# Optimization experiments

Hardware: AMD Instinct MI355X
Metric: run time of the kernel (lower is better)

Reference implementation:

```python
import jax, jax.numpy as jnp
import numpy as np

NUM_HEADS = 16


def setup_inputs() -> dict:
    key = jax.random.key(0)
    ks = jax.random.split(key, 5)
    B, N, D = 2, 2048, 1024
    scale = 1.0 / np.sqrt(D)  # roughly xavier-ish magnitude for weights
    return {
        "x": jax.random.normal(ks[0], (B, N, D), dtype=jnp.float32),
        "W_query": jax.random.normal(ks[1], (D, D), dtype=jnp.float32) * scale,
        "W_key": jax.random.normal(ks[2], (D, D), dtype=jnp.float32) * scale,
        "W_value": jax.random.normal(ks[3], (D, D), dtype=jnp.float32) * scale,
        "W_output": jax.random.normal(ks[4], (D, D), dtype=jnp.float32) * scale,
    }


def reference(x, W_query, W_key, W_value, W_output):
    # x: [B, N, D]; weights: [D, D]
    B, N, D = x.shape
    H = NUM_HEADS
    hd = D // H

    def mh_embed(W):
        # linear_embedding then split heads: [B, N, D] -> [B, H, N, hd]
        y = jnp.einsum("bnd,de->bne", x, W)
        return y.reshape(B, N, H, hd).transpose(0, 2, 1, 3)

    q = mh_embed(W_query)
    k = mh_embed(W_key)
    v = mh_embed(W_value)

    # NOTE: source scales by token_dim**-0.5 (full model dim), not head_dim
    attn = jnp.einsum("bhnd,bhmd->bhnm", q, k) * (D ** -0.5)
    attn = jax.nn.softmax(attn, axis=-1)
    out = jnp.einsum("bhnm,bhmd->bhnd", attn, v)  # [B, H, N, hd]

    out = out.transpose(0, 2, 1, 3).reshape(B, N, D)  # merge heads
    out = jnp.einsum("bnd,de->bne", out, W_output)
    return out
```

## Files before the change

kernel.cpp:

```cpp
#include <hip/hip_runtime.h>

#define D_MODEL 1024
#define N_TOK   2048
#define NHEAD   16
#define HDIM    64
#define BATCH   2
#define M_TOT   (BATCH*N_TOK)

typedef unsigned short u16;
typedef __bf16 bf16x8 __attribute__((ext_vector_type(8)));
typedef float  f32x4  __attribute__((ext_vector_type(4)));

#define QSCALE 0.04508422002777439f

__device__ __forceinline__ u16 f2bf(float f) {
  union { float f; unsigned u; } v; v.f = f;
  unsigned r = v.u + 0x7fffu + ((v.u >> 16) & 1u);
  return (u16)(r >> 16);
}

__device__ __forceinline__ unsigned pk2bf(float a, float b) {
#if __has_builtin(__builtin_amdgcn_cvt_pk_bf16_f32)
  typedef __bf16 bf16x2_t __attribute__((ext_vector_type(2)));
  bf16x2_t r = __builtin_amdgcn_cvt_pk_bf16_f32(a, b);
  union { bf16x2_t v; unsigned u; } c; c.v = r; return c.u;
#else
  return (unsigned)f2bf(a) | ((unsigned)f2bf(b) << 16);
#endif
}

__device__ __forceinline__ void gl2lds16(const void* g, void* l) {
  __builtin_amdgcn_global_load_lds(
      (__attribute__((address_space(1))) void*)g,
      (__attribute__((address_space(3))) void*)l, 16, 0, 0);
}

__global__ void prep_kernel(const float* __restrict__ x,
                            const float* __restrict__ s0, const float* __restrict__ s1,
                            const float* __restrict__ s2, const float* __restrict__ s3,
                            u16* __restrict__ xb,
                            u16* __restrict__ d0, u16* __restrict__ d1,
                            u16* __restrict__ d2, u16* __restrict__ d3) {
  const int t = threadIdx.y * 32 + threadIdx.x;
  if (blockIdx.z == 4) {
    int base = (blockIdx.y * 32 + blockIdx.x) * 256 + t;
#pragma unroll
    for (int r = 0; r < 4; ++r) {
      int i = base + r * 262144;
      float4 v = ((const float4*)x)[i];
      ushort4 o;
      o.x = f2bf(v.x); o.y = f2bf(v.y); o.z = f2bf(v.z); o.w = f2bf(v.w);
      ((ushort4*)xb)[i] = o;
    }
    return;
  }
  const float* src; u16* dst;
  switch (blockIdx.z) {
    case 0:  src = s0; dst = d0; break;
    case 1:  src = s1; dst = d1; break;
    case 2:  src = s2; dst = d2; break;
    default: src = s3; dst = d3; break;
  }
  float sc = (blockIdx.z == 0) ? QSCALE : 1.0f;
  __shared__ float tile[32][33];
  int xg = blockIdx.x * 32 + threadIdx.x;
  int ybase = blockIdx.y * 32;
#pragma unroll
  for (int r = 0; r < 4; ++r)
    tile[threadIdx.y + r*8][threadIdx.x] = src[(size_t)(ybase + threadIdx.y + r*8)*D_MODEL + xg];
  __syncthreads();
#pragma unroll
  for (int r = 0; r < 4; ++r)
    dst[(size_t)(blockIdx.x*32 + threadIdx.y + r*8)*D_MODEL + ybase + threadIdx.x] =
        f2bf(tile[threadIdx.x][threadIdx.y + r*8] * sc);
}

__device__ __forceinline__ void gemm_body(const u16* __restrict__ A,
                                          const u16* __restrict__ Bt,
                                          void* __restrict__ Cout, int mode) {
  __shared__ __attribute__((aligned(16))) u16 lA[2][128*32];
  __shared__ __attribute__((aligned(16))) u16 lB[2][128*32];
  const int t = threadIdx.x;
  const int lane = t & 63, w = t >> 6;
  const int wm = w >> 1, wn = w & 1;
  const int q4 = lane >> 4, l15 = lane & 15;
  const int m0 = blockIdx.y * 128, n0 = blockIdx.x * 128;

  const int c0 = t, c1 = 256 + t;
  const int r0 = c0 >> 2, g0 = (c0 & 3) ^ (r0 & 3);
  const int r1 = c1 >> 2, g1 = (c1 & 3) ^ (r1 & 3);

  f32x4 acc[4][4] = {};

  gl2lds16(A  + (size_t)(m0 + r0)*D_MODEL + g0*8, &lA[0][c0*8]);
  gl2lds16(Bt + (size_t)(n0 + r0)*D_MODEL + g0*8, &lB[0][c0*8]);
  gl2lds16(A  + (size_t)(m0 + r1)*D_MODEL + g1*8, &lA[0][c1*8]);
  gl2lds16(Bt + (size_t)(n0 + r1)*D_MODEL + g1*8, &lB[0][c1*8]);

  for (int it = 0; it < 32; ++it) {
    const int cur = it & 1;
    __syncthreads();
    if (it + 1 < 32) {
      const int kn = (it + 1) * 32;
      u16* dA = &lA[cur ^ 1][0]; u16* dB = &lB[cur ^ 1][0];
      gl2lds16(A  + (size_t)(m0 + r0)*D_MODEL + kn + g0*8, dA + c0*8);
      gl2lds16(Bt + (size_t)(n0 + r0)*D_MODEL + kn + g0*8, dB + c0*8);
      gl2lds16(A  + (size_t)(m0 + r1)*D_MODEL + kn + g1*8, dA + c1*8);
      gl2lds16(Bt + (size_t)(n0 + r1)*D_MODEL + kn + g1*8, dB + c1*8);
    }
    const u16* sA = &lA[cur][0]; const u16* sB = &lB[cur][0];
    bf16x8 af[4], bfr[4];
#pragma unroll
    for (int mi = 0; mi < 4; ++mi) {
      int r = wm*64 + mi*16 + l15;
      af[mi] = *(const bf16x8*)(sA + r*32 + ((q4 ^ (r & 3)) * 8));
    }
#pragma unroll
    for (int ni = 0; ni < 4; ++ni) {
      int r = wn*64 + ni*16 + l15;
      bfr[ni] = *(const bf16x8*)(sB + r*32 + ((q4 ^ (r & 3)) * 8));
    }
#pragma unroll
    for (int mi = 0; mi < 4; ++mi)
#pragma unroll
      for (int ni = 0; ni < 4; ++ni)
        acc[mi][ni] = __builtin_amdgcn_mfma_f32_16x16x32_bf16(af[mi], bfr[ni], acc[mi][ni], 0, 0, 0);
  }

#pragma unroll
  for (int mi = 0; mi < 4; ++mi) {
#pragma unroll
    for (int ni = 0; ni < 4; ++ni) {
      const int tok0 = m0 + wm*64 + mi*16 + q4*4;
      const int col  = n0 + wn*64 + ni*16 + l15;
      if (mode == 0) {
        u16* D = (u16*)Cout;
#pragma unroll
        for (int r = 0; r < 4; ++r) {
          int tok = tok0 + r;
          int b = tok >> 11, n = tok & (N_TOK-1);
          int h = col >> 6, d = col & (HDIM-1);
          D[(((size_t)(b*NHEAD + h))*N_TOK + n)*HDIM + d] = f2bf(acc[mi][ni][r]);
        }
      } else if (mode == 2) {
        int b = tok0 >> 11, n = tok0 & (N_TOK-1);
        int h = col >> 6, d = col & (HDIM-1);
        ushort4 pk;
        pk.x = f2bf(acc[mi][ni][0]); pk.y = f2bf(acc[mi][ni][1]);
        pk.z = f2bf(acc[mi][ni][2]); pk.w = f2bf(acc[mi][ni][3]);
        *(ushort4*)((u16*)Cout + ((size_t)(b*NHEAD + h)*HDIM + d)*N_TOK + n) = pk;
      } else {
        float* D = (float*)Cout;
#pragma unroll
        for (int r = 0; r < 4; ++r)
          D[(size_t)(tok0 + r)*D_MODEL + col] = acc[mi][ni][r];
      }
    }
  }
}

__global__ __launch_bounds__(256) void qkv_kernel(const u16* __restrict__ xb,
    const u16* __restrict__ wqt, const u16* __restrict__ wkt, const u16* __restrict__ wvt,
    u16* __restrict__ Q, u16* __restrict__ K, u16* __restrict__ Vt) {
  int z = blockIdx.z;
  const u16* B = (z == 0) ? wqt : (z == 1) ? wkt : wvt;
  void* C = (z == 0) ? (void*)Q : (z == 1) ? (void*)K : (void*)Vt;
  gemm_body(xb, B, C, (z == 2) ? 2 : 0);
}

__global__ __launch_bounds__(256) void out_kernel(const u16* __restrict__ ctx,
    const u16* __restrict__ wot, float* __restrict__ out) {
  gemm_body(ctx, wot, (void*)out, 3);
}

__global__ __launch_bounds__(256, 3) void attn_kernel(const u16* __restrict__ Qg,
    const u16* __restrict__ Kg, const u16* __restrict__ Vtg,
    float* __restrict__ Opart, float* __restrict__ Lpart) {
  __shared__ __attribute__((aligned(16))) u16 lds[24576];
  const int t = threadIdx.x;
  const int lane = t & 63, w = t >> 6;
  const int q4 = lane >> 4, l15 = lane & 15;
  const int bh = blockIdx.y;
  const int qb = blockIdx.x >> 1, half = blockIdx.x & 1;
  const int qw0 = qb * 128 + w * 32;
  const size_t kvBase = (size_t)bh * (N_TOK * HDIM);
  u16* myP = lds + 16384 + w * 2048;

  const int ck0 = t, ck1 = 256 + t;
  const int kr0 = ck0 >> 3, kg0 = (ck0 & 7) ^ (kr0 & 7);
  const int kr1 = ck1 >> 3, kg1 = (ck1 & 7) ^ (kr1 & 7);

  bf16x8 qf[2][2];
#pragma unroll
  for (int ni = 0; ni < 2; ++ni)
#pragma unroll
    for (int kk = 0; kk < 2; ++kk)
      qf[ni][kk] = *(const bf16x8*)(Qg + kvBase +
                    (size_t)(qw0 + ni*16 + l15)*HDIM + kk*32 + q4*8);

  f32x4 accO[4][2] = {};
  float lsum[2] = {0.f, 0.f};

  const int kvStart = half * 1024;
  gl2lds16(Kg  + kvBase + (size_t)(kvStart + kr0)*HDIM + kg0*8, lds + ck0*8);
  gl2lds16(Kg  + kvBase + (size_t)(kvStart + kr1)*HDIM + kg1*8, lds + ck1*8);
  gl2lds16(Vtg + kvBase + (size_t)kr0*N_TOK + kvStart + kg0*8,  lds + 8192 + ck0*8);
  gl2lds16(Vtg + kvBase + (size_t)kr1*N_TOK + kvStart + kg1*8,  lds + 8192 + ck1*8);

  for (int it = 0; it < 16; ++it) {
    const int cur = it & 1;
    __syncthreads();
    if (it + 1 < 16) {
      const int kvn = kvStart + (it + 1) * 64;
      u16* dK = lds + (cur ^ 1) * 4096;
      u16* dV = lds + 8192 + (cur ^ 1) * 4096;
      gl2lds16(Kg  + kvBase + (size_t)(kvn + kr0)*HDIM + kg0*8, dK + ck0*8);
      gl2lds16(Kg  + kvBase + (size_t)(kvn + kr1)*HDIM + kg1*8, dK + ck1*8);
      gl2lds16(Vtg + kvBase + (size_t)kr0*N_TOK + kvn + kg0*8,  dV + ck0*8);
      gl2lds16(Vtg + kvBase + (size_t)kr1*N_TOK + kvn + kg1*8,  dV + ck1*8);
    }
    const u16* sK = lds + cur * 4096;
    const u16* sV = lds + 8192 + cur * 4096;

#pragma unroll
    for (int mip = 0; mip < 4; ++mip) {
      const int kv = mip*16 + l15;
      f32x4 s[2] = {};
#pragma unroll
      for (int kk = 0; kk < 2; ++kk) {
        bf16x8 a = *(const bf16x8*)(sK + kv*64 + (((kk*4 + q4) ^ (l15 & 7)) * 8));
#pragma unroll
        for (int ni = 0; ni < 2; ++ni)
          s[ni] = __builtin_amdgcn_mfma_f32_16x16x32_bf16(a, qf[ni][kk], s[ni], 0, 0, 0);
      }
#pragma unroll
      for (int ni = 0; ni < 2; ++ni) {
        float p0 = __builtin_amdgcn_exp2f(s[ni][0]);
        float p1 = __builtin_amdgcn_exp2f(s[ni][1]);
        float p2 = __builtin_amdgcn_exp2f(s[ni][2]);
        float p3 = __builtin_amdgcn_exp2f(s[ni][3]);
        lsum[ni] += (p0 + p1) + (p2 + p3);
        uint2 u; u.x = pk2bf(p0, p1); u.y = pk2bf(p2, p3);
        const int qloc = ni*16 + l15;
        const int kv8 = mip*4 + q4;
        *(uint2*)(myP + qloc*64 + (((kv8 >> 1) ^ (qloc & 7)) * 8) + (kv8 & 1)*4) = u;
      }
    }

#pragma unroll
    for (int kk2 = 0; kk2 < 2; ++kk2) {
      bf16x8 bp[2];
#pragma unroll
      for (int ni = 0; ni < 2; ++ni)
        bp[ni] = *(const bf16x8*)(myP + (ni*16 + l15)*64 +
                                  (((kk2*4 + q4) ^ (l15 & 7)) * 8));
#pragma unroll
      for (int mi2 = 0; mi2 < 4; ++mi2) {
        const int d = mi2*16 + l15;
        bf16x8 av = *(const bf16x8*)(sV + d*64 + (((kk2*4 + q4) ^ (d & 7)) * 8));
#pragma unroll
        for (int ni = 0; ni < 2; ++ni)
          accO[mi2][ni] = __builtin_amdgcn_mfma_f32_16x16x32_bf16(av, bp[ni], accO[mi2][ni], 0, 0, 0);
      }
    }
  }

  const int b = bh >> 4, head = bh & (NHEAD-1);
  float* Obase = Opart + (size_t)half * (M_TOT * D_MODEL);
#pragma unroll
  for (int ni = 0; ni < 2; ++ni) {
    float ls = lsum[ni];
    ls += __shfl_xor(ls, 16);
    ls += __shfl_xor(ls, 32);
    const int q = qw0 + ni*16 + l15;
    if (q4 == 0)
      Lpart[(size_t)half*(32*N_TOK) + bh*N_TOK + q] = ls;
    const size_t rb = ((size_t)(b*N_TOK + q))*D_MODEL + head*HDIM + q4*4;
#pragma unroll
    for (int mi2 = 0; mi2 < 4; ++mi2) {
      float4 v;
      v.x = accO[mi2][ni][0]; v.y = accO[mi2][ni][1];
      v.z = accO[mi2][ni][2]; v.w = accO[mi2][ni][3];
      *(float4*)(Obase + rb + mi2*16) = v;
    }
  }
}

__global__ __launch_bounds__(256) void combine_kernel(const float* __restrict__ Opart,
    const float* __restrict__ Lpart, u16* __restrict__ ctx) {
  int i = blockIdx.x * 256 + threadIdx.x;
  int tok = i >> 8, d4 = i & 255;
  int n = tok & (N_TOK-1), b = tok >> 11;
  int h = d4 >> 4;
  int bh = b*NHEAD + h;
  float l = Lpart[(size_t)bh*N_TOK + n] + Lpart[(size_t)(32*N_TOK) + bh*N_TOK + n];
  float inv = 1.0f / l;
  float4 o0 = *(const float4*)(Opart + (size_t)tok*D_MODEL + d4*4);
  float4 o1 = *(const float4*)(Opart + (size_t)(M_TOT*D_MODEL) + (size_t)tok*D_MODEL + d4*4);
  ushort4 o;
  o.x = f2bf((o0.x + o1.x) * inv);
  o.y = f2bf((o0.y + o1.y) * inv);
  o.z = f2bf((o0.z + o1.z) * inv);
  o.w = f2bf((o0.w + o1.w) * inv);
  *(ushort4*)(ctx + (size_t)tok*D_MODEL + d4*4) = o;
}

extern "C" void kernel_launch(void* const* d_in, const int* in_sizes, int n_in,
                              void* d_out, int out_size, void* d_ws, size_t ws_size,
                              hipStream_t stream) {
  const float* x  = (const float*)d_in[0];
  const float* Wq = (const float*)d_in[1];
  const float* Wk = (const float*)d_in[2];
  const float* Wv = (const float*)d_in[3];
  const float* Wo = (const float*)d_in[4];
  float* out = (float*)d_out;

  char* ws = (char*)d_ws;
  u16* xb   = (u16*)(ws);
  u16* wqt  = (u16*)(ws + (8u  << 20));
  u16* wkt  = (u16*)(ws + (10u << 20));
  u16* wvt  = (u16*)(ws + (12u << 20));
  u16* wot  = (u16*)(ws + (14u << 20));
  u16* Qw   = (u16*)(ws + (16u << 20));
  u16* Kw   = (u16*)(ws + (24u << 20));
  u16* Vtw  = (u16*)(ws + (32u << 20));
  u16* ctx  = (u16*)(ws + (40u << 20));
  float* Op = (float*)(ws + (48u << 20));
  float* Lp = (float*)(ws + (80u << 20));
  (void)in_sizes; (void)n_in; (void)out_size; (void)ws_size;

  prep_kernel<<<dim3(32, 32, 5), dim3(32, 8), 0, stream>>>(x, Wq, Wk, Wv, Wo,
                                                           xb, wqt, wkt, wvt, wot);
  qkv_kernel<<<dim3(8, 32, 3), 256, 0, stream>>>(xb, wqt, wkt, wvt, Qw, Kw, Vtw);
  attn_kernel<<<dim3(32, 32), 256, 0, stream>>>(Qw, Kw, Vtw, Op, Lp);
  combine_kernel<<<4096, 256, 0, stream>>>(Op, Lp, ctx);
  out_kernel<<<dim3(8, 32), 256, 0, stream>>>(ctx, wot, out);
}
```

Measured before the change: 204.5 us.

## Store attention partials in bf16 and give output GEMM its own smaller tile

The attention kernel now writes its split-KV partial outputs as bf16 instead of fp32, which halves the partial-buffer traffic. The combine kernel reads the bf16 partials and handles 8 elements per thread. The output projection gets a dedicated kernel with 64x128 tiles and double-buffered LDS, so it launches twice as many blocks for better occupancy on the GPU. The cost is extra bf16 rounding of the unnormalized partial sums before they are combined.

```diff
diff --git a/kernel.cpp b/kernel.cpp
--- a/kernel.cpp
+++ b/kernel.cpp
@@ -17,6 +17,10 @@
   union { float f; unsigned u; } v; v.f = f;
   unsigned r = v.u + 0x7fffu + ((v.u >> 16) & 1u);
   return (u16)(r >> 16);
+}
+
+__device__ __forceinline__ float bf2f(u16 u) {
+  union { unsigned u; float f; } v; v.u = ((unsigned)u) << 16; return v.f;
 }
 
 __device__ __forceinline__ unsigned pk2bf(float a, float b) {
@@ -142,18 +146,13 @@
           int h = col >> 6, d = col & (HDIM-1);
           D[(((size_t)(b*NHEAD + h))*N_TOK + n)*HDIM + d] = f2bf(acc[mi][ni][r]);
         }
-      } else if (mode == 2) {
+      } else {
         int b = tok0 >> 11, n = tok0 & (N_TOK-1);
         int h = col >> 6, d = col & (HDIM-1);
         ushort4 pk;
         pk.x = f2bf(acc[mi][ni][0]); pk.y = f2bf(acc[mi][ni][1]);
         pk.z = f2bf(acc[mi][ni][2]); pk.w = f2bf(acc[mi][ni][3]);
         *(ushort4*)((u16*)Cout + ((size_t)(b*NHEAD + h)*HDIM + d)*N_TOK + n) = pk;
-      } else {
-        float* D = (float*)Cout;
-#pragma unroll
-        for (int r = 0; r < 4; ++r)
-          D[(size_t)(tok0 + r)*D_MODEL + col] = acc[mi][ni][r];
       }
     }
   }
@@ -170,12 +169,70 @@
 
 __global__ __launch_bounds__(256) void out_kernel(const u16* __restrict__ ctx,
     const u16* __restrict__ wot, float* __restrict__ out) {
-  gemm_body(ctx, wot, (void*)out, 3);
+  __shared__ __attribute__((aligned(16))) u16 lA[2][64*32];
+  __shared__ __attribute__((aligned(16))) u16 lB[2][128*32];
+  const int t = threadIdx.x;
+  const int lane = t & 63, w = t >> 6;
+  const int wm = w >> 1, wn = w & 1;
+  const int q4 = lane >> 4, l15 = lane & 15;
+  const int m0 = blockIdx.y * 64, n0 = blockIdx.x * 128;
+
+  const int rA = t >> 2, gA = (t & 3) ^ (rA & 3);
+  const int c0 = t, c1 = 256 + t;
+  const int r0 = c0 >> 2, g0 = (c0 & 3) ^ (r0 & 3);
+  const int r1 = c1 >> 2, g1 = (c1 & 3) ^ (r1 & 3);
+
+  f32x4 acc[2][4] = {};
+
+  gl2lds16(ctx + (size_t)(m0 + rA)*D_MODEL + gA*8, &lA[0][t*8]);
+  gl2lds16(wot + (size_t)(n0 + r0)*D_MODEL + g0*8, &lB[0][c0*8]);
+  gl2lds16(wot + (size_t)(n0 + r1)*D_MODEL + g1*8, &lB[0][c1*8]);
+
+  for (int it = 0; it < 32; ++it) {
+    const int cur = it & 1;
+    __syncthreads();
+    if (it + 1 < 32) {
+      const int kn = (it + 1) * 32;
+      u16* dA = &lA[cur ^ 1][0]; u16* dB = &lB[cur ^ 1][0];
+      gl2lds16(ctx + (size_t)(m0 + rA)*D_MODEL + kn + gA*8, dA + t*8);
+      gl2lds16(wot + (size_t)(n0 + r0)*D_MODEL + kn + g0*8, dB + c0*8);
+      gl2lds16(wot + (size_t)(n0 + r1)*D_MODEL + kn + g1*8, dB + c1*8);
+    }
+    const u16* sA = &lA[cur][0]; const u16* sB = &lB[cur][0];
+    bf16x8 af[2], bfr[4];
+#pragma unroll
+    for (int mi = 0; mi < 2; ++mi) {
+      int r = wm*32 + mi*16 + l15;
+      af[mi] = *(const bf16x8*)(sA + r*32 + ((q4 ^ (r & 3)) * 8));
+    }
+#pragma unroll
+    for (int ni = 0; ni < 4; ++ni) {
+      int r = wn*64 + ni*16 + l15;
+      bfr[ni] = *(const bf16x8*)(sB + r*32 + ((q4 ^ (r & 3)) * 8));
+    }
+#pragma unroll
+    for (int mi = 0; mi < 2; ++mi)
+#pragma unroll
+      for (int ni = 0; ni < 4; ++ni)
+        acc[mi][ni] = __builtin_amdgcn_mfma_f32_16x16x32_bf16(af[mi], bfr[ni], acc[mi][ni], 0, 0, 0);
+  }
+
+#pragma unroll
+  for (int mi = 0; mi < 2; ++mi) {
+#pragma unroll
+    for (int ni = 0; ni < 4; ++ni) {
+      const int tok0 = m0 + wm*32 + mi*16 + q4*4;
+      const int col  = n0 + wn*64 + ni*16 + l15;
+#pragma unroll
+      for (int r = 0; r < 4; ++r)
+        out[(size_t)(tok0 + r)*D_MODEL + col] = acc[mi][ni][r];
+    }
+  }
 }
 
 __global__ __launch_bounds__(256, 3) void attn_kernel(const u16* __restrict__ Qg,
     const u16* __restrict__ Kg, const u16* __restrict__ Vtg,
-    float* __restrict__ Opart, float* __restrict__ Lpart) {
+    u16* __restrict__ Opart, float* __restrict__ Lpart) {
   __shared__ __attribute__((aligned(16))) u16 lds[24576];
   const int t = threadIdx.x;
   const int lane = t & 63, w = t >> 6;
@@ -266,7 +323,7 @@
   }
 
   const int b = bh >> 4, head = bh & (NHEAD-1);
-  float* Obase = Opart + (size_t)half * (M_TOT * D_MODEL);
+  u16* Obase = Opart + (size_t)half * (M_TOT * D_MODEL);
 #pragma unroll
   for (int ni = 0; ni < 2; ++ni) {
     float ls = lsum[ni];
@@ -278,31 +335,35 @@
     const size_t rb = ((size_t)(b*N_TOK + q))*D_MODEL + head*HDIM + q4*4;
 #pragma unroll
     for (int mi2 = 0; mi2 < 4; ++mi2) {
-      float4 v;
-      v.x = accO[mi2][ni][0]; v.y = accO[mi2][ni][1];
-      v.z = accO[mi2][ni][2]; v.w = accO[mi2][ni][3];
-      *(float4*)(Obase + rb + mi2*16) = v;
-    }
-  }
-}
-
-__global__ __launch_bounds__(256) void combine_kernel(const float* __restrict__ Opart,
+      uint2 u;
+      u.x = pk2bf(accO[mi2][ni][0], accO[mi2][ni][1]);
+      u.y = pk2bf(accO[mi2][ni][2], accO[mi2][ni][3]);
+      *(uint2*)(Obase + rb + mi2*16) = u;
+    }
+  }
+}
+
+__global__ __launch_bounds__(256) void combine_kernel(const u16* __restrict__ Opart,
     const float* __restrict__ Lpart, u16* __restrict__ ctx) {
   int i = blockIdx.x * 256 + threadIdx.x;
-  int tok = i >> 8, d4 = i & 255;
+  int tok = i >> 7, c8 = i & 127;
   int n = tok & (N_TOK-1), b = tok >> 11;
-  int h = d4 >> 4;
+  int h = c8 >> 3;
   int bh = b*NHEAD + h;
   float l = Lpart[(size_t)bh*N_TOK + n] + Lpart[(size_t)(32*N_TOK) + bh*N_TOK + n];
   float inv = 1.0f / l;
-  float4 o0 = *(const float4*)(Opart + (size_t)tok*D_MODEL + d4*4);
-  float4 o1 = *(const float4*)(Opart + (size_t)(M_TOT*D_MODEL) + (size_t)tok*D_MODEL + d4*4);
-  ushort4 o;
-  o.x = f2bf((o0.x + o1.x) * inv);
-  o.y = f2bf((o0.y + o1.y) * inv);
-  o.z = f2bf((o0.z + o1.z) * inv);
-  o.w = f2bf((o0.w + o1.w) * inv);
-  *(ushort4*)(ctx + (size_t)tok*D_MODEL + d4*4) = o;
+  const size_t off = (size_t)tok*D_MODEL + c8*8;
+  ushort4 a0 = *(const ushort4*)(Opart + off);
+  ushort4 a1 = *(const ushort4*)(Opart + off + 4);
+  ushort4 b0 = *(const ushort4*)(Opart + (size_t)(M_TOT*D_MODEL) + off);
+  ushort4 b1 = *(const ushort4*)(Opart + (size_t)(M_TOT*D_MODEL) + off + 4);
+  uint2 o0, o1;
+  o0.x = pk2bf((bf2f(a0.x)+bf2f(b0.x))*inv, (bf2f(a0.y)+bf2f(b0.y))*inv);
+  o0.y = pk2bf((bf2f(a0.z)+bf2f(b0.z))*inv, (bf2f(a0.w)+bf2f(b0.w))*inv);
+  o1.x = pk2bf((bf2f(a1.x)+bf2f(b1.x))*inv, (bf2f(a1.y)+bf2f(b1.y))*inv);
+  o1.y = pk2bf((bf2f(a1.z)+bf2f(b1.z))*inv, (bf2f(a1.w)+bf2f(b1.w))*inv);
+  *(uint2*)(ctx + off) = o0;
+  *(uint2*)(ctx + off + 4) = o1;
 }
 
 extern "C" void kernel_launch(void* const* d_in, const int* in_sizes, int n_in,
@@ -325,14 +386,14 @@
   u16* Kw   = (u16*)(ws + (24u << 20));
   u16* Vtw  = (u16*)(ws + (32u << 20));
   u16* ctx  = (u16*)(ws + (40u << 20));
-  float* Op = (float*)(ws + (48u << 20));
-  float* Lp = (float*)(ws + (80u << 20));
+  u16* Op   = (u16*)(ws + (48u << 20));
+  float* Lp = (float*)(ws + (64u << 20));
   (void)in_sizes; (void)n_in; (void)out_size; (void)ws_size;
 
   prep_kernel<<<dim3(32, 32, 5), dim3(32, 8), 0, stream>>>(x, Wq, Wk, Wv, Wo,
                                                            xb, wqt, wkt, wvt, wot);
   qkv_kernel<<<dim3(8, 32, 3), 256, 0, stream>>>(xb, wqt, wkt, wvt, Qw, Kw, Vtw);
   attn_kernel<<<dim3(32, 32), 256, 0, stream>>>(Qw, Kw, Vtw, Op, Lp);
-  combine_kernel<<<4096, 256, 0, stream>>>(Op, Lp, ctx);
-  out_kernel<<<dim3(8, 32), 256, 0, stream>>>(ctx, wot, out);
-}
+  combine_kernel<<<2048, 256, 0, stream>>>(Op, Lp, ctx);
+  out_kernel<<<dim3(8, 64), 256, 0, stream>>>(ctx, wot, out);
+}
```

Result: no change. 201.5 us (-1.4%).
